# Optimization experiments

Measured on AMD Instinct MI355X. Metric: run time of the kernel, lower is better.

## Reference

```python
import jax, jax.numpy as jnp
import numpy as np

DEPTH = 10
N_VARS = 2
BATCH = 32768
N_LEAVES = 2 ** DEPTH
N_INTERNAL = N_LEAVES - 1
TAU = 1.0
# fp32 analogues of torch.finfo(float64).eps based guards
EPS = float(np.finfo(np.float32).eps)      # _TERM_EPS / _CHILD_EPS
BYPASS = 1.0 - EPS                          # _BYPASS
CLAMP = 1e30                                # _CLAMP (fp32-safe)
TERM_R, TERM_I = 1.0, 0.0                   # EML terminal '1' -> 1+0j
CHILD_IDX = N_VARS + 1


def setup_inputs() -> dict:
    key = jax.random.key(0)
    k1, k2, k3 = jax.random.split(key, 3)
    x = jax.random.normal(k1, (BATCH, N_VARS), dtype=jnp.float32)
    leaf_logits = jax.random.normal(k2, (N_LEAVES, N_VARS + 1), dtype=jnp.float32)
    leaf_logits = leaf_logits.at[:, 0].add(2.0)
    gate_logits = jax.random.normal(k3, (N_INTERNAL, 2, N_VARS + 2), dtype=jnp.float32)
    gate_logits = gate_logits.at[..., 0].add(4.0)
    return {"x": x, "leaf_logits": leaf_logits, "gate_logits": gate_logits}


def _clamp_complex(z):
    r = jnp.clip(jnp.nan_to_num(z.real, nan=0.0, posinf=CLAMP, neginf=-CLAMP), -CLAMP, CLAMP)
    i = jnp.clip(jnp.nan_to_num(z.imag, nan=0.0, posinf=CLAMP, neginf=-CLAMP), -CLAMP, CLAMP)
    return jax.lax.complex(r, i)


def _blend(ps, child, x_r, x_i):
    # ps: [n_pairs, n_vars+2], child: [B, n_pairs] complex
    p_child = ps[:, CHILD_IDX][None, :]                      # [1, P]
    mask_c = p_child > EPS
    safe_cr = jnp.where(mask_c, child.real, 0.0)
    safe_ci = jnp.where(mask_c, child.imag, 0.0)
    p_child_safe = jnp.where(mask_c, p_child, 0.0)
    p_term = ps[:, 0][None, :]                               # [1, P]
    # variable contributions: [P, V] x [B, V] -> [B, P]
    var_r = jnp.einsum('pv,bv->bp', ps[:, 1:CHILD_IDX], x_r)
    var_i = jnp.einsum('pv,bv->bp', ps[:, 1:CHILD_IDX], x_i)
    blend_r = p_term * TERM_R + p_child_safe * safe_cr + var_r
    blend_i = p_term * TERM_I + p_child_safe * safe_ci + var_i
    # hard bypass when one prob saturates
    b1 = p_term > BYPASS
    blend_r = jnp.where(b1, TERM_R, blend_r)
    blend_i = jnp.where(b1, TERM_I, blend_i)
    for v in range(N_VARS):
        bx = ps[:, v + 1][None, :] > BYPASS
        blend_r = jnp.where(bx, x_r[:, v:v + 1], blend_r)
        blend_i = jnp.where(bx, x_i[:, v:v + 1], blend_i)
    return jax.lax.complex(blend_r, blend_i)


def reference(x, leaf_logits, gate_logits):
    xc = x.astype(jnp.complex64)                              # [B, V]
    batch = x.shape[0]
    w = jax.nn.softmax(leaf_logits / TAU, axis=1).astype(jnp.complex64)  # [L, V+1]
    term_col = jnp.full((batch, 1), TERM_R + 0j, dtype=jnp.complex64)
    candidates = jnp.concatenate([term_col, xc], axis=1)      # [B, V+1]
    level = candidates @ w.T                                  # [B, L]
    gate_probs = jax.nn.softmax(gate_logits / TAU, axis=-1)   # [I, 2, V+2]
    x_r, x_i = x, jnp.zeros_like(x)

    node_idx = 0
    while level.shape[1] > 1:  # static python loop over DEPTH levels
        n_pairs = level.shape[1] // 2
        left = level[:, 0::2]
        right = level[:, 1::2]
        pg = gate_probs[node_idx:node_idx + n_pairs]          # [P, 2, V+2]
        left_in = _blend(pg[:, 0, :], left, x_r, x_i)
        right_in = _blend(pg[:, 1, :], right, x_r, x_i)
        # EML op: eml(a, b) = exp(a) - ln(b)
        level = _clamp_complex(jnp.exp(left_in) - jnp.log(right_in))
        node_idx += n_pairs

    leaf_probs = jax.nn.softmax(leaf_logits / TAU, axis=1)
    return level[:, 0], leaf_probs, gate_probs
```

## Files before the change

kernel.cpp:

```cpp
#include <hip/hip_runtime.h>
#include <math.h>

#define EPSF     1.1920928955078125e-07f
#define BYPASSF  0.9999998807907104f
#define CLAMPF   1e30f
#define NBATCH   32768

#define INV2PI    0.15915494309189535f
#define INV2PI_HI 0.15915493667125701904f
#define INV2PI_LO 6.42063831e-9f
#define L2E       1.4426950408889634f
#define L2E_HI    1.44269502162933349609f
#define L2E_LO    1.92596299e-8f
#define LN2F      0.69314718055994530942f
#define PI_F      3.14159274101257324219f
#define PIO2_F    1.57079637050628662109f

#define SLAB_SRC 504
#define SLAB_LDS 508
#define GDS_FLOATS (16 * SLAB_LDS + 120)
#define LW_F4_STRIDE 65
#define WS_NEED ((4096 + 8184) * 4)

typedef float v2 __attribute__((ext_vector_type(2)));

__device__ __attribute__((noinline)) float2 slow_sincos(float y) {
  return make_float2(sinf(y), cosf(y));
}

__device__ __forceinline__ void softmax3_store(float a, float b, float c, float* out) {
  float m = fmaxf(a, fmaxf(b, c));
  float e0 = expf(a - m), e1 = expf(b - m), e2 = expf(c - m);
  float s = (e0 + e1) + e2;
  out[0] = e0 / s; out[1] = e1 / s; out[2] = e2 / s;
}

__device__ __forceinline__ void softmax4(const float* __restrict__ in, float* out) {
  float a = in[0], b = in[1], c = in[2], d = in[3];
  float m = fmaxf(fmaxf(a, b), fmaxf(c, d));
  float e0 = expf(a - m), e1 = expf(b - m), e2 = expf(c - m), e3 = expf(d - m);
  float s = ((e0 + e1) + e2) + e3;
  out[0] = e0 / s; out[1] = e1 / s; out[2] = e2 / s; out[3] = e3 / s;
}

__device__ __forceinline__ void fold_gate(float* p) {
  if (p[3] <= EPSF) p[3] = 0.0f;
  if (p[0] > BYPASSF)      { p[0]=1.f; p[1]=0.f; p[2]=0.f; p[3]=0.f; }
  else if (p[1] > BYPASSF) { p[0]=0.f; p[1]=1.f; p[2]=0.f; p[3]=0.f; }
  else if (p[2] > BYPASSF) { p[0]=0.f; p[1]=0.f; p[2]=1.f; p[3]=0.f; }
}

__device__ __forceinline__ float exp_core(float xe, int* n_out) {
  float nf = rintf(xe * L2E);
  float f  = fmaf(xe, L2E_HI, -nf);
  f        = fmaf(xe, L2E_LO, f);
  *n_out   = (int)nf;
  return __builtin_amdgcn_exp2f(f);
}

__device__ __forceinline__ v2 combine2(const float* __restrict__ g8, v2 L, v2 R,
                                       float x0, float x1) {
  float4 gl = *(const float4*)(g8);
  float4 gr = *(const float4*)(g8 + 4);
  float cL = fmaf(gl.z, x1, gl.y * x0) + gl.x;
  float cR = fmaf(gr.z, x1, gr.y * x0) + gr.x;
  v2 lin = __builtin_elementwise_fma((v2){gl.w, gl.w}, L, (v2){cL, 0.0f});
  v2 rin = __builtin_elementwise_fma((v2){gr.w, gr.w}, R, (v2){cR, 0.0f});

  float sy, cy;
  {
    float nf = rintf(lin.y * INV2PI);
    float rv = fmaf(lin.y, INV2PI_HI, -nf);
    rv       = fmaf(lin.y, INV2PI_LO, rv);
    sy = __builtin_amdgcn_sinf(rv);
    cy = __builtin_amdgcn_cosf(rv);
    if (fabsf(lin.y) > 20000.0f) { float2 sc = slow_sincos(lin.y); sy = sc.x; cy = sc.y; }
  }

  float xe = fminf(fmaxf(lin.x, -200.0f), 200.0f);
  int ne;
  float eh = exp_core(xe, &ne);
  v2 ecs = (v2){eh, eh} * (v2){cy, sy};
  float er = __builtin_amdgcn_ldexpf(ecs.x, ne);
  float ei = __builtin_amdgcn_ldexpf(ecs.y, ne);

  float ax = fabsf(rin.x), ay = fabsf(rin.y);
  float mx = fmaxf(ax, ay), mn = fminf(ax, ay);
  float s  = (mx == 0.0f) ? 0.0f : mn * __builtin_amdgcn_rcpf(mx);
  float z  = s * s;
  float lr = LN2F * fmaf(0.5f, __builtin_amdgcn_logf(z + 1.0f), __builtin_amdgcn_logf(mx));
  float u =              0.00282363896f;
  u = fmaf(u, z, -0.0159569028f);
  u = fmaf(u, z,  0.0425049886f);
  u = fmaf(u, z, -0.0748900920f);
  u = fmaf(u, z,  0.1063479334f);
  u = fmaf(u, z, -0.1420273631f);
  u = fmaf(u, z,  0.1999269574f);
  u = fmaf(u, z, -0.3333310186f);
  float at = fmaf(s * z, u, s);
  at = (ay > ax)      ? (PIO2_F - at) : at;
  at = (rin.x < 0.0f) ? (PI_F   - at) : at;
  float li = copysignf(at, rin.y);

  v2 d = (v2){er, ei} - (v2){lr, li};
  v2 c = __builtin_elementwise_min(__builtin_elementwise_max(d, (v2)(-CLAMPF)), (v2)(CLAMPF));
  v2 o;
  o.x = (d.x != d.x) ? 0.0f : c.x;
  o.y = (d.y != d.y) ? 0.0f : c.y;
  return o;
}

__device__ __forceinline__ v2 combine_l1(const float* __restrict__ g8, float Lr, float Rr,
                                         float x0, float x1) {
  float4 gl = *(const float4*)(g8);
  float4 gr = *(const float4*)(g8 + 4);
  float lr_ = fmaf(gl.w, Lr, fmaf(gl.z, x1, gl.y * x0) + gl.x);
  float rr_ = fmaf(gr.w, Rr, fmaf(gr.z, x1, gr.y * x0) + gr.x);

  float xe = fminf(fmaxf(lr_, -200.0f), 200.0f);
  int ne;
  float eh = exp_core(xe, &ne);
  float er = __builtin_amdgcn_ldexpf(eh, ne);

  float lr = LN2F * __builtin_amdgcn_logf(fabsf(rr_));
  v2 o;
  o.x = fminf(fmaxf(er - lr, -CLAMPF), CLAMPF);
  o.y = (rr_ < 0.0f) ? -PI_F : 0.0f;
  return o;
}

__device__ __forceinline__ v2 quartet(const float* __restrict__ bp, const float4* __restrict__ lq,
                                      float x0, float x1) {
  float4 w0 = lq[0], w1 = lq[1], w2 = lq[2], w3 = lq[3];
  float a0 = fmaf(w0.z, x1, fmaf(w0.y, x0, w0.x));
  float a1 = fmaf(w1.z, x1, fmaf(w1.y, x0, w1.x));
  float a2 = fmaf(w2.z, x1, fmaf(w2.y, x0, w2.x));
  float a3 = fmaf(w3.z, x1, fmaf(w3.y, x0, w3.x));
  v2 c01 = combine_l1(bp + 0, a0, a1, x0, x1);
  v2 c23 = combine_l1(bp + 8, a2, a3, x0, x1);
  return combine2(bp + 16, c01, c23, x0, x1);
}

__global__ __launch_bounds__(256) void prep_kernel(
    const float* __restrict__ leaf_logits,
    const float* __restrict__ gate_logits,
    float* __restrict__ out_leaf,
    float* __restrict__ out_gate,
    float* __restrict__ ws_leaf,
    float* __restrict__ ws_gate) {
  int i = blockIdx.x * 256 + threadIdx.x;
  if (i < 1024) {
    float p[3];
    softmax3_store(leaf_logits[i * 3], leaf_logits[i * 3 + 1], leaf_logits[i * 3 + 2], p);
    out_leaf[i * 3] = p[0]; out_leaf[i * 3 + 1] = p[1]; out_leaf[i * 3 + 2] = p[2];
    ((float4*)ws_leaf)[i] = make_float4(p[0], p[1], p[2], 0.0f);
  } else if (i < 1024 + 2046) {
    int j = i - 1024;
    int g = j >> 1, half = j & 1;
    float p[4];
    softmax4(gate_logits + j * 4, p);
    ((float4*)out_gate)[j] = make_float4(p[0], p[1], p[2], p[3]);
    fold_gate(p);
    int di;
    if (g < 1008) {
      int z  = 1024 - g;
      int k  = __clz(z - 1) - 21;
      int pp = g - (1024 - (2048 >> k));
      int t  = pp >> (6 - k);
      int pl = pp & ((1 << (6 - k)) - 1);
      int L  = ((pl + 1) << k) - 1;
      int step = L - __popc(L) + (k - 1);
      di = t * SLAB_SRC + step * 8;
    } else {
      di = 16 * SLAB_SRC + (g - 1008) * 8;
    }
    ((float4*)(ws_gate + di))[half] = make_float4(p[0], p[1], p[2], p[3]);
  }
}

__global__ __launch_bounds__(1024, 2) void tree16_kernel(
    const float* __restrict__ x,
    const float* __restrict__ ws_leaf,
    const float* __restrict__ ws_gate,
    float* __restrict__ out0, int cplx) {

  __shared__ __align__(16) float gds[GDS_FLOATS];
  __shared__ __align__(16) float lwds[16 * LW_F4_STRIDE * 4];
  const int tid = threadIdx.x;

  {
    float4* g4 = (float4*)gds;
    const float4* s4 = (const float4*)ws_gate;
    for (int c = tid; c < 2016; c += 1024) {
      int t = c / 126;
      int r = c - t * 126;
      g4[t * 127 + r] = s4[c];
    }
    if (tid < 30) g4[2032 + tid] = s4[2016 + tid];
    float4* l4 = (float4*)lwds;
    const float4* sl = (const float4*)ws_leaf;
    l4[tid + (tid >> 6)] = sl[tid];
  }
  __syncthreads();

  const int gtid = blockIdx.x * 1024 + tid;
  const int e  = gtid >> 4;
  const int lt = tid & 15;
  const float2 xv = ((const float2*)x)[e];
  const float x0 = xv.x, x1 = xv.y;
  const float* gb  = &gds[lt * SLAB_LDS];
  const float* tds = &gds[16 * SLAB_LDS];
  const float4* lwp = (const float4*)lwds + lt * LW_F4_STRIDE;

  v2 p4, p5, p6;
  v2 res = (v2)(0.0f);
  int off = 0;

  #pragma unroll 1
  for (int h2 = 0; h2 < 8; ++h2) {
    const float* bp = gb + off;
    const float4* lq = lwp + 8 * h2;
    v2 c03 = quartet(bp +  0, lq,     x0, x1);
    v2 c47 = quartet(bp + 24, lq + 4, x0, x1);
    v2 cur = combine2(bp + 48, c03, c47, x0, x1);
    if (!(h2 & 1)) { p4 = cur; }
    else {
      cur = combine2(bp + 56, p4, cur, x0, x1);
      if (!(h2 & 2)) { p5 = cur; }
      else {
        cur = combine2(bp + 64, p5, cur, x0, x1);
        if (!(h2 & 4)) { p6 = cur; }
        else           { res = combine2(bp + 72, p6, cur, x0, x1); }
      }
    }
    off = (8 * (h2 + 1) - __popc(h2 + 1)) * 8;
  }

  v2 v = res;
  { v2 o; o.x = __shfl_xor(v.x, 1); o.y = __shfl_xor(v.y, 1);
    v2 L, R;
    L.x = (lt & 1) ? o.x : v.x; L.y = (lt & 1) ? o.y : v.y;
    R.x = (lt & 1) ? v.x : o.x; R.y = (lt & 1) ? v.y : o.y;
    v = combine2(tds + (lt >> 1) * 8, L, R, x0, x1); }
  { v2 o; o.x = __shfl_xor(v.x, 2); o.y = __shfl_xor(v.y, 2);
    v2 L, R;
    L.x = (lt & 2) ? o.x : v.x; L.y = (lt & 2) ? o.y : v.y;
    R.x = (lt & 2) ? v.x : o.x; R.y = (lt & 2) ? v.y : o.y;
    v = combine2(tds + (8 + (lt >> 2)) * 8, L, R, x0, x1); }
  { v2 o; o.x = __shfl_xor(v.x, 4); o.y = __shfl_xor(v.y, 4);
    v2 L, R;
    L.x = (lt & 4) ? o.x : v.x; L.y = (lt & 4) ? o.y : v.y;
    R.x = (lt & 4) ? v.x : o.x; R.y = (lt & 4) ? v.y : o.y;
    v = combine2(tds + (12 + (lt >> 3)) * 8, L, R, x0, x1); }
  { v2 o; o.x = __shfl_xor(v.x, 8); o.y = __shfl_xor(v.y, 8);
    v2 L, R;
    L.x = (lt & 8) ? o.x : v.x; L.y = (lt & 8) ? o.y : v.y;
    R.x = (lt & 8) ? v.x : o.x; R.y = (lt & 8) ? v.y : o.y;
    v = combine2(tds + 14 * 8, L, R, x0, x1); }

  if (lt == 0) {
    if (cplx) { out0[2 * e] = v.x; out0[2 * e + 1] = v.y; }
    else      { out0[e] = v.x; }
  }
}

#define GSTRIDE  1020
#define LSTRIDE  516

__device__ __forceinline__ void store_gate_fb(const float* __restrict__ in, float* __restrict__ out) {
  float p[4];
  softmax4(in, p);
  fold_gate(p);
  out[0]=p[0]; out[1]=p[1]; out[2]=p[2]; out[3]=p[3];
}

__global__ __launch_bounds__(512) void tree_fb_kernel(
    const float* __restrict__ x,
    const float* __restrict__ leaf_logits,
    const float* __restrict__ gate_logits,
    float* __restrict__ out0, int cplx) {

  __shared__ __align__(16) float gds[8 * GSTRIDE];
  __shared__ __align__(16) float tds[7 * 8];
  __shared__ __align__(16) float lw[8 * LSTRIDE];
  const int tid = threadIdx.x;

  for (int l = tid; l < 1024; l += 512) {
    float p[3];
    softmax3_store(leaf_logits[l * 3], leaf_logits[l * 3 + 1], leaf_logits[l * 3 + 2], p);
    *(float4*)&lw[(l >> 7) * LSTRIDE + (l & 127) * 4] = make_float4(p[0], p[1], p[2], 0.0f);
  }
  for (int g = tid; g < 1016; g += 512) {
    int z  = 1024 - g;
    int k  = __clz(z - 1) - 21;
    int p  = g - (1024 - (2048 >> k));
    int t  = p >> (7 - k);
    int pl = p & ((1 << (7 - k)) - 1);
    int L  = ((pl + 1) << k) - 1;
    int step = L - __popc(L) + (k - 1);
    float* dst = &gds[t * GSTRIDE + step * 8];
    store_gate_fb(gate_logits + g * 8,     dst);
    store_gate_fb(gate_logits + g * 8 + 4, dst + 4);
  }
  if (tid < 7) {
    int g = 1016 + tid;
    store_gate_fb(gate_logits + g * 8,     &tds[tid * 8]);
    store_gate_fb(gate_logits + g * 8 + 4, &tds[tid * 8 + 4]);
  }
  __syncthreads();

  const int gtid = blockIdx.x * 512 + tid;
  const int e  = gtid >> 3;
  const int lt = tid & 7;
  const float2 xv = ((const float2*)x)[e];
  const float x0 = xv.x, x1 = xv.y;
  const float* gb = &gds[lt * GSTRIDE];
  const float* lb = &lw[lt * LSTRIDE];

  v2 p1, p2, p3, p4, p5, p6;
  v2 res = (v2)(0.0f);
  int step = 0;

  #pragma unroll 2
  for (int h = 0; h < 64; ++h) {
    float4 w0 = *(const float4*)&lb[(2 * h) * 4];
    float4 w1 = *(const float4*)&lb[(2 * h + 1) * 4];
    float a = fmaf(w0.z, x1, fmaf(w0.y, x0, w0.x));
    float b = fmaf(w1.z, x1, fmaf(w1.y, x0, w1.x));
    v2 cur = combine_l1(gb + step * 8, a, b, x0, x1); step++;
    if (!(h & 1))  { p1 = cur; continue; }
    cur = combine2(gb + step * 8, p1, cur, x0, x1); step++;
    if (!(h & 2))  { p2 = cur; continue; }
    cur = combine2(gb + step * 8, p2, cur, x0, x1); step++;
    if (!(h & 4))  { p3 = cur; continue; }
    cur = combine2(gb + step * 8, p3, cur, x0, x1); step++;
    if (!(h & 8))  { p4 = cur; continue; }
    cur = combine2(gb + step * 8, p4, cur, x0, x1); step++;
    if (!(h & 16)) { p5 = cur; continue; }
    cur = combine2(gb + step * 8, p5, cur, x0, x1); step++;
    if (!(h & 32)) { p6 = cur; continue; }
    cur = combine2(gb + step * 8, p6, cur, x0, x1); step++;
    res = cur;
  }

  v2 v = res;
  { v2 o; o.x = __shfl_xor(v.x, 1); o.y = __shfl_xor(v.y, 1);
    v2 L, R;
    L.x = (lt & 1) ? o.x : v.x; L.y = (lt & 1) ? o.y : v.y;
    R.x = (lt & 1) ? v.x : o.x; R.y = (lt & 1) ? v.y : o.y;
    v = combine2(&tds[(lt >> 1) * 8], L, R, x0, x1); }
  { v2 o; o.x = __shfl_xor(v.x, 2); o.y = __shfl_xor(v.y, 2);
    v2 L, R;
    L.x = (lt & 2) ? o.x : v.x; L.y = (lt & 2) ? o.y : v.y;
    R.x = (lt & 2) ? v.x : o.x; R.y = (lt & 2) ? v.y : o.y;
    v = combine2(&tds[(4 + (lt >> 2)) * 8], L, R, x0, x1); }
  { v2 o; o.x = __shfl_xor(v.x, 4); o.y = __shfl_xor(v.y, 4);
    v2 L, R;
    L.x = (lt & 4) ? o.x : v.x; L.y = (lt & 4) ? o.y : v.y;
    R.x = (lt & 4) ? v.x : o.x; R.y = (lt & 4) ? v.y : o.y;
    v = combine2(&tds[6 * 8], L, R, x0, x1); }

  if (lt == 0) {
    if (cplx) { out0[2 * e] = v.x; out0[2 * e + 1] = v.y; }
    else      { out0[e] = v.x; }
  }
}

__global__ __launch_bounds__(256) void probs_fb_kernel(
    const float* __restrict__ leaf_logits,
    const float* __restrict__ gate_logits,
    float* __restrict__ out_leaf,
    float* __restrict__ out_gate) {
  int i = blockIdx.x * 256 + threadIdx.x;
  if (i < 1024) {
    softmax3_store(leaf_logits[i * 3], leaf_logits[i * 3 + 1], leaf_logits[i * 3 + 2],
                   &out_leaf[i * 3]);
  } else if (i < 1024 + 2046) {
    int j = i - 1024;
    float p[4];
    softmax4(gate_logits + j * 4, p);
    ((float4*)out_gate)[j] = make_float4(p[0], p[1], p[2], p[3]);
  }
}

extern "C" void kernel_launch(void* const* d_in, const int* in_sizes, int n_in,
                              void* d_out, int out_size, void* d_ws, size_t ws_size,
                              hipStream_t stream) {
  const float* x  = (const float*)d_in[0];
  const float* ll = (const float*)d_in[1];
  const float* gl = (const float*)d_in[2];
  float* out0 = (float*)d_out;

  int S = out_size - (3072 + 8184);
  int cplx = (S >= 2 * NBATCH) ? 1 : 0;
  float* out_leaf = out0 + S;
  float* out_gate = out_leaf + 3072;

  if (ws_size >= (size_t)WS_NEED) {
    float* ws_leaf = (float*)d_ws;
    float* ws_gate = ws_leaf + 4096;
    prep_kernel<<<12, 256, 0, stream>>>(ll, gl, out_leaf, out_gate, ws_leaf, ws_gate);
    tree16_kernel<<<512, 1024, 0, stream>>>(x, ws_leaf, ws_gate, out0, cplx);
  } else {
    tree_fb_kernel<<<512, 512, 0, stream>>>(x, ll, gl, out0, cplx);
    probs_fb_kernel<<<12, 256, 0, stream>>>(ll, gl, out_leaf, out_gate);
  }
}
```

Measured before the change: 55.57 us.

## Process two batch elements per thread with packed float2 math in tree kernel

New measurement: 50.93 us. 1.09x faster.

```diff
diff --git a/kernel.cpp b/kernel.cpp
--- a/kernel.cpp
+++ b/kernel.cpp
@@ -24,6 +24,12 @@
 
 typedef float v2 __attribute__((ext_vector_type(2)));
 
+__device__ __forceinline__ v2 pkfma(v2 a, v2 b, v2 c) {
+  return __builtin_elementwise_fma(a, b, c);
+}
+
+struct C2p { v2 r, i; };
+
 __device__ __attribute__((noinline)) float2 slow_sincos(float y) {
   return make_float2(sinf(y), cosf(y));
 }
@@ -50,95 +56,120 @@
   else if (p[2] > BYPASSF) { p[0]=0.f; p[1]=0.f; p[2]=1.f; p[3]=0.f; }
 }
 
-__device__ __forceinline__ float exp_core(float xe, int* n_out) {
-  float nf = rintf(xe * L2E);
-  float f  = fmaf(xe, L2E_HI, -nf);
-  f        = fmaf(xe, L2E_LO, f);
-  *n_out   = (int)nf;
-  return __builtin_amdgcn_exp2f(f);
-}
-
-__device__ __forceinline__ v2 combine2(const float* __restrict__ g8, v2 L, v2 R,
-                                       float x0, float x1) {
+
+__device__ __forceinline__ C2p combine2p(const float* __restrict__ g8, C2p L, C2p R,
+                                         v2 x0, v2 x1) {
   float4 gl = *(const float4*)(g8);
   float4 gr = *(const float4*)(g8 + 4);
-  float cL = fmaf(gl.z, x1, gl.y * x0) + gl.x;
-  float cR = fmaf(gr.z, x1, gr.y * x0) + gr.x;
-  v2 lin = __builtin_elementwise_fma((v2){gl.w, gl.w}, L, (v2){cL, 0.0f});
-  v2 rin = __builtin_elementwise_fma((v2){gr.w, gr.w}, R, (v2){cR, 0.0f});
-
-  float sy, cy;
+  v2 cL = pkfma((v2)(gl.z), x1, (v2)(gl.y) * x0) + (v2)(gl.x);
+  v2 cR = pkfma((v2)(gr.z), x1, (v2)(gr.y) * x0) + (v2)(gr.x);
+  v2 linr = pkfma((v2)(gl.w), L.r, cL);
+  v2 lini = (v2)(gl.w) * L.i;
+  v2 rinr = pkfma((v2)(gr.w), R.r, cR);
+  v2 rini = (v2)(gr.w) * R.i;
+
+  v2 sy, cy;
   {
-    float nf = rintf(lin.y * INV2PI);
-    float rv = fmaf(lin.y, INV2PI_HI, -nf);
-    rv       = fmaf(lin.y, INV2PI_LO, rv);
-    sy = __builtin_amdgcn_sinf(rv);
-    cy = __builtin_amdgcn_cosf(rv);
-    if (fabsf(lin.y) > 20000.0f) { float2 sc = slow_sincos(lin.y); sy = sc.x; cy = sc.y; }
-  }
-
-  float xe = fminf(fmaxf(lin.x, -200.0f), 200.0f);
-  int ne;
-  float eh = exp_core(xe, &ne);
-  v2 ecs = (v2){eh, eh} * (v2){cy, sy};
-  float er = __builtin_amdgcn_ldexpf(ecs.x, ne);
-  float ei = __builtin_amdgcn_ldexpf(ecs.y, ne);
-
-  float ax = fabsf(rin.x), ay = fabsf(rin.y);
-  float mx = fmaxf(ax, ay), mn = fminf(ax, ay);
-  float s  = (mx == 0.0f) ? 0.0f : mn * __builtin_amdgcn_rcpf(mx);
-  float z  = s * s;
-  float lr = LN2F * fmaf(0.5f, __builtin_amdgcn_logf(z + 1.0f), __builtin_amdgcn_logf(mx));
-  float u =              0.00282363896f;
-  u = fmaf(u, z, -0.0159569028f);
-  u = fmaf(u, z,  0.0425049886f);
-  u = fmaf(u, z, -0.0748900920f);
-  u = fmaf(u, z,  0.1063479334f);
-  u = fmaf(u, z, -0.1420273631f);
-  u = fmaf(u, z,  0.1999269574f);
-  u = fmaf(u, z, -0.3333310186f);
-  float at = fmaf(s * z, u, s);
-  at = (ay > ax)      ? (PIO2_F - at) : at;
-  at = (rin.x < 0.0f) ? (PI_F   - at) : at;
-  float li = copysignf(at, rin.y);
-
-  v2 d = (v2){er, ei} - (v2){lr, li};
-  v2 c = __builtin_elementwise_min(__builtin_elementwise_max(d, (v2)(-CLAMPF)), (v2)(CLAMPF));
-  v2 o;
-  o.x = (d.x != d.x) ? 0.0f : c.x;
-  o.y = (d.y != d.y) ? 0.0f : c.y;
+    v2 t = lini * (v2)(INV2PI);
+    v2 nf; nf.x = rintf(t.x); nf.y = rintf(t.y);
+    v2 rv = pkfma(lini, (v2)(INV2PI_HI), -nf);
+    rv     = pkfma(lini, (v2)(INV2PI_LO), rv);
+    sy.x = __builtin_amdgcn_sinf(rv.x); sy.y = __builtin_amdgcn_sinf(rv.y);
+    cy.x = __builtin_amdgcn_cosf(rv.x); cy.y = __builtin_amdgcn_cosf(rv.y);
+    if (fabsf(lini.x) > 20000.0f) { float2 sc = slow_sincos(lini.x); sy.x = sc.x; cy.x = sc.y; }
+    if (fabsf(lini.y) > 20000.0f) { float2 sc = slow_sincos(lini.y); sy.y = sc.x; cy.y = sc.y; }
+  }
+
+  v2 xe; xe.x = __builtin_amdgcn_fmed3f(linr.x, -200.0f, 200.0f);
+         xe.y = __builtin_amdgcn_fmed3f(linr.y, -200.0f, 200.0f);
+  v2 t2 = xe * (v2)(L2E);
+  v2 nfe; nfe.x = rintf(t2.x); nfe.y = rintf(t2.y);
+  v2 f = pkfma(xe, (v2)(L2E_HI), -nfe);
+  f     = pkfma(xe, (v2)(L2E_LO), f);
+  v2 eh; eh.x = __builtin_amdgcn_exp2f(f.x); eh.y = __builtin_amdgcn_exp2f(f.y);
+  int ne0 = (int)nfe.x, ne1 = (int)nfe.y;
+  v2 ecr = eh * cy, eci = eh * sy;
+  v2 er, ei;
+  er.x = __builtin_amdgcn_ldexpf(ecr.x, ne0); er.y = __builtin_amdgcn_ldexpf(ecr.y, ne1);
+  ei.x = __builtin_amdgcn_ldexpf(eci.x, ne0); ei.y = __builtin_amdgcn_ldexpf(eci.y, ne1);
+
+  v2 mx, mn;
+  mx.x = fmaxf(fabsf(rinr.x), fabsf(rini.x)); mx.y = fmaxf(fabsf(rinr.y), fabsf(rini.y));
+  mn.x = fminf(fabsf(rinr.x), fabsf(rini.x)); mn.y = fminf(fabsf(rinr.y), fabsf(rini.y));
+  v2 rc; rc.x = __builtin_amdgcn_rcpf(mx.x); rc.y = __builtin_amdgcn_rcpf(mx.y);
+  v2 s = mn * rc;
+  s.x = (mx.x == 0.0f) ? 0.0f : s.x;
+  s.y = (mx.y == 0.0f) ? 0.0f : s.y;
+  v2 z = s * s;
+  v2 lga; lga.x = __builtin_amdgcn_logf(z.x + 1.0f); lga.y = __builtin_amdgcn_logf(z.y + 1.0f);
+  v2 lgm; lgm.x = __builtin_amdgcn_logf(mx.x);       lgm.y = __builtin_amdgcn_logf(mx.y);
+  v2 lr = (v2)(LN2F) * pkfma((v2)(0.5f), lga, lgm);
+  v2 u = (v2)(0.00282363896f);
+  u = pkfma(u, z, (v2)(-0.0159569028f));
+  u = pkfma(u, z, (v2)( 0.0425049886f));
+  u = pkfma(u, z, (v2)(-0.0748900920f));
+  u = pkfma(u, z, (v2)( 0.1063479334f));
+  u = pkfma(u, z, (v2)(-0.1420273631f));
+  u = pkfma(u, z, (v2)( 0.1999269574f));
+  u = pkfma(u, z, (v2)(-0.3333310186f));
+  v2 at = pkfma(s * z, u, s);
+  v2 q1 = (v2)(PIO2_F) - at;
+  at.x = (fabsf(rini.x) > fabsf(rinr.x)) ? q1.x : at.x;
+  at.y = (fabsf(rini.y) > fabsf(rinr.y)) ? q1.y : at.y;
+  v2 q2 = (v2)(PI_F) - at;
+  at.x = (rinr.x < 0.0f) ? q2.x : at.x;
+  at.y = (rinr.y < 0.0f) ? q2.y : at.y;
+  v2 li; li.x = copysignf(at.x, rini.x); li.y = copysignf(at.y, rini.y);
+
+  v2 dre = er - lr, dim = ei - li;
+  v2 cre = __builtin_elementwise_min(__builtin_elementwise_max(dre, (v2)(-CLAMPF)), (v2)(CLAMPF));
+  v2 cim = __builtin_elementwise_min(__builtin_elementwise_max(dim, (v2)(-CLAMPF)), (v2)(CLAMPF));
+  C2p o;
+  o.r.x = (dre.x != dre.x) ? 0.0f : cre.x;
+  o.r.y = (dre.y != dre.y) ? 0.0f : cre.y;
+  o.i.x = (dim.x != dim.x) ? 0.0f : cim.x;
+  o.i.y = (dim.y != dim.y) ? 0.0f : cim.y;
   return o;
 }
 
-__device__ __forceinline__ v2 combine_l1(const float* __restrict__ g8, float Lr, float Rr,
-                                         float x0, float x1) {
+__device__ __forceinline__ C2p combine_l1p(const float* __restrict__ g8, v2 Lr, v2 Rr,
+                                           v2 x0, v2 x1) {
   float4 gl = *(const float4*)(g8);
   float4 gr = *(const float4*)(g8 + 4);
-  float lr_ = fmaf(gl.w, Lr, fmaf(gl.z, x1, gl.y * x0) + gl.x);
-  float rr_ = fmaf(gr.w, Rr, fmaf(gr.z, x1, gr.y * x0) + gr.x);
-
-  float xe = fminf(fmaxf(lr_, -200.0f), 200.0f);
-  int ne;
-  float eh = exp_core(xe, &ne);
-  float er = __builtin_amdgcn_ldexpf(eh, ne);
-
-  float lr = LN2F * __builtin_amdgcn_logf(fabsf(rr_));
-  v2 o;
-  o.x = fminf(fmaxf(er - lr, -CLAMPF), CLAMPF);
-  o.y = (rr_ < 0.0f) ? -PI_F : 0.0f;
+  v2 lr_ = pkfma((v2)(gl.w), Lr, pkfma((v2)(gl.z), x1, (v2)(gl.y) * x0) + (v2)(gl.x));
+  v2 rr_ = pkfma((v2)(gr.w), Rr, pkfma((v2)(gr.z), x1, (v2)(gr.y) * x0) + (v2)(gr.x));
+
+  v2 xe; xe.x = __builtin_amdgcn_fmed3f(lr_.x, -200.0f, 200.0f);
+         xe.y = __builtin_amdgcn_fmed3f(lr_.y, -200.0f, 200.0f);
+  v2 t2 = xe * (v2)(L2E);
+  v2 nfe; nfe.x = rintf(t2.x); nfe.y = rintf(t2.y);
+  v2 f = pkfma(xe, (v2)(L2E_HI), -nfe);
+  f     = pkfma(xe, (v2)(L2E_LO), f);
+  v2 eh; eh.x = __builtin_amdgcn_exp2f(f.x); eh.y = __builtin_amdgcn_exp2f(f.y);
+  v2 er;
+  er.x = __builtin_amdgcn_ldexpf(eh.x, (int)nfe.x);
+  er.y = __builtin_amdgcn_ldexpf(eh.y, (int)nfe.y);
+
+  v2 lg; lg.x = __builtin_amdgcn_logf(fabsf(rr_.x)); lg.y = __builtin_amdgcn_logf(fabsf(rr_.y));
+  v2 d = er - (v2)(LN2F) * lg;
+  C2p o;
+  o.r.x = __builtin_amdgcn_fmed3f(d.x, -CLAMPF, CLAMPF);
+  o.r.y = __builtin_amdgcn_fmed3f(d.y, -CLAMPF, CLAMPF);
+  o.i.x = (rr_.x < 0.0f) ? -PI_F : 0.0f;
+  o.i.y = (rr_.y < 0.0f) ? -PI_F : 0.0f;
   return o;
 }
 
-__device__ __forceinline__ v2 quartet(const float* __restrict__ bp, const float4* __restrict__ lq,
-                                      float x0, float x1) {
+__device__ __forceinline__ C2p quartetp(const float* __restrict__ bp, const float4* __restrict__ lq,
+                                        v2 x0, v2 x1) {
   float4 w0 = lq[0], w1 = lq[1], w2 = lq[2], w3 = lq[3];
-  float a0 = fmaf(w0.z, x1, fmaf(w0.y, x0, w0.x));
-  float a1 = fmaf(w1.z, x1, fmaf(w1.y, x0, w1.x));
-  float a2 = fmaf(w2.z, x1, fmaf(w2.y, x0, w2.x));
-  float a3 = fmaf(w3.z, x1, fmaf(w3.y, x0, w3.x));
-  v2 c01 = combine_l1(bp + 0, a0, a1, x0, x1);
-  v2 c23 = combine_l1(bp + 8, a2, a3, x0, x1);
-  return combine2(bp + 16, c01, c23, x0, x1);
+  v2 a0 = pkfma((v2)(w0.z), x1, pkfma((v2)(w0.y), x0, (v2)(w0.x)));
+  v2 a1 = pkfma((v2)(w1.z), x1, pkfma((v2)(w1.y), x0, (v2)(w1.x)));
+  v2 a2 = pkfma((v2)(w2.z), x1, pkfma((v2)(w2.y), x0, (v2)(w2.x)));
+  v2 a3 = pkfma((v2)(w3.z), x1, pkfma((v2)(w3.y), x0, (v2)(w3.x)));
+  C2p c01 = combine_l1p(bp + 0, a0, a1, x0, x1);
+  C2p c23 = combine_l1p(bp + 8, a2, a3, x0, x1);
+  return combine2p(bp + 16, c01, c23, x0, x1);
 }
 
 __global__ __launch_bounds__(256) void prep_kernel(
@@ -178,7 +209,7 @@
   }
 }
 
-__global__ __launch_bounds__(1024, 2) void tree16_kernel(
+__global__ __launch_bounds__(1024, 1) void tree16p_kernel(
     const float* __restrict__ x,
     const float* __restrict__ ws_leaf,
     const float* __restrict__ ws_gate,
@@ -204,68 +235,157 @@
   __syncthreads();
 
   const int gtid = blockIdx.x * 1024 + tid;
-  const int e  = gtid >> 4;
+  const int pe = gtid >> 4;
   const int lt = tid & 15;
-  const float2 xv = ((const float2*)x)[e];
-  const float x0 = xv.x, x1 = xv.y;
+  const float4 xw = ((const float4*)x)[pe];
+  v2 x0, x1;
+  x0.x = xw.x; x0.y = xw.z;
+  x1.x = xw.y; x1.y = xw.w;
   const float* gb  = &gds[lt * SLAB_LDS];
   const float* tds = &gds[16 * SLAB_LDS];
   const float4* lwp = (const float4*)lwds + lt * LW_F4_STRIDE;
 
-  v2 p4, p5, p6;
-  v2 res = (v2)(0.0f);
+  C2p p4, p5, p6;
+  C2p res; res.r = (v2)(0.0f); res.i = (v2)(0.0f);
   int off = 0;
 
   #pragma unroll 1
   for (int h2 = 0; h2 < 8; ++h2) {
     const float* bp = gb + off;
     const float4* lq = lwp + 8 * h2;
-    v2 c03 = quartet(bp +  0, lq,     x0, x1);
-    v2 c47 = quartet(bp + 24, lq + 4, x0, x1);
-    v2 cur = combine2(bp + 48, c03, c47, x0, x1);
+    C2p c03 = quartetp(bp +  0, lq,     x0, x1);
+    C2p c47 = quartetp(bp + 24, lq + 4, x0, x1);
+    C2p cur = combine2p(bp + 48, c03, c47, x0, x1);
     if (!(h2 & 1)) { p4 = cur; }
     else {
-      cur = combine2(bp + 56, p4, cur, x0, x1);
+      cur = combine2p(bp + 56, p4, cur, x0, x1);
       if (!(h2 & 2)) { p5 = cur; }
       else {
-        cur = combine2(bp + 64, p5, cur, x0, x1);
+        cur = combine2p(bp + 64, p5, cur, x0, x1);
         if (!(h2 & 4)) { p6 = cur; }
-        else           { res = combine2(bp + 72, p6, cur, x0, x1); }
+        else           { res = combine2p(bp + 72, p6, cur, x0, x1); }
       }
     }
     off = (8 * (h2 + 1) - __popc(h2 + 1)) * 8;
   }
 
-  v2 v = res;
-  { v2 o; o.x = __shfl_xor(v.x, 1); o.y = __shfl_xor(v.y, 1);
-    v2 L, R;
-    L.x = (lt & 1) ? o.x : v.x; L.y = (lt & 1) ? o.y : v.y;
-    R.x = (lt & 1) ? v.x : o.x; R.y = (lt & 1) ? v.y : o.y;
-    v = combine2(tds + (lt >> 1) * 8, L, R, x0, x1); }
-  { v2 o; o.x = __shfl_xor(v.x, 2); o.y = __shfl_xor(v.y, 2);
-    v2 L, R;
-    L.x = (lt & 2) ? o.x : v.x; L.y = (lt & 2) ? o.y : v.y;
-    R.x = (lt & 2) ? v.x : o.x; R.y = (lt & 2) ? v.y : o.y;
-    v = combine2(tds + (8 + (lt >> 2)) * 8, L, R, x0, x1); }
-  { v2 o; o.x = __shfl_xor(v.x, 4); o.y = __shfl_xor(v.y, 4);
-    v2 L, R;
-    L.x = (lt & 4) ? o.x : v.x; L.y = (lt & 4) ? o.y : v.y;
-    R.x = (lt & 4) ? v.x : o.x; R.y = (lt & 4) ? v.y : o.y;
-    v = combine2(tds + (12 + (lt >> 3)) * 8, L, R, x0, x1); }
-  { v2 o; o.x = __shfl_xor(v.x, 8); o.y = __shfl_xor(v.y, 8);
-    v2 L, R;
-    L.x = (lt & 8) ? o.x : v.x; L.y = (lt & 8) ? o.y : v.y;
-    R.x = (lt & 8) ? v.x : o.x; R.y = (lt & 8) ? v.y : o.y;
-    v = combine2(tds + 14 * 8, L, R, x0, x1); }
+  C2p v = res;
+  { C2p o;
+    o.r.x = __shfl_xor(v.r.x, 1); o.r.y = __shfl_xor(v.r.y, 1);
+    o.i.x = __shfl_xor(v.i.x, 1); o.i.y = __shfl_xor(v.i.y, 1);
+    bool sw = (lt & 1);
+    C2p L, R;
+    L.r = sw ? o.r : v.r; L.i = sw ? o.i : v.i;
+    R.r = sw ? v.r : o.r; R.i = sw ? v.i : o.i;
+    v = combine2p(tds + (lt >> 1) * 8, L, R, x0, x1); }
+  { C2p o;
+    o.r.x = __shfl_xor(v.r.x, 2); o.r.y = __shfl_xor(v.r.y, 2);
+    o.i.x = __shfl_xor(v.i.x, 2); o.i.y = __shfl_xor(v.i.y, 2);
+    bool sw = (lt & 2);
+    C2p L, R;
+    L.r = sw ? o.r : v.r; L.i = sw ? o.i : v.i;
+    R.r = sw ? v.r : o.r; R.i = sw ? v.i : o.i;
+    v = combine2p(tds + (8 + (lt >> 2)) * 8, L, R, x0, x1); }
+  { C2p o;
+    o.r.x = __shfl_xor(v.r.x, 4); o.r.y = __shfl_xor(v.r.y, 4);
+    o.i.x = __shfl_xor(v.i.x, 4); o.i.y = __shfl_xor(v.i.y, 4);
+    bool sw = (lt & 4);
+    C2p L, R;
+    L.r = sw ? o.r : v.r; L.i = sw ? o.i : v.i;
+    R.r = sw ? v.r : o.r; R.i = sw ? v.i : o.i;
+    v = combine2p(tds + (12 + (lt >> 3)) * 8, L, R, x0, x1); }
+  { C2p o;
+    o.r.x = __shfl_xor(v.r.x, 8); o.r.y = __shfl_xor(v.r.y, 8);
+    o.i.x = __shfl_xor(v.i.x, 8); o.i.y = __shfl_xor(v.i.y, 8);
+    bool sw = (lt & 8);
+    C2p L, R;
+    L.r = sw ? o.r : v.r; L.i = sw ? o.i : v.i;
+    R.r = sw ? v.r : o.r; R.i = sw ? v.i : o.i;
+    v = combine2p(tds + 14 * 8, L, R, x0, x1); }
 
   if (lt == 0) {
-    if (cplx) { out0[2 * e] = v.x; out0[2 * e + 1] = v.y; }
-    else      { out0[e] = v.x; }
+    if (cplx) {
+      ((float4*)out0)[pe] = make_float4(v.r.x, v.i.x, v.r.y, v.i.y);
+    } else {
+      ((float2*)out0)[pe] = make_float2(v.r.x, v.r.y);
+    }
   }
 }
 
 #define GSTRIDE  1020
 #define LSTRIDE  516
+
+__device__ __forceinline__ v2 combine2(const float* __restrict__ g8, v2 L, v2 R,
+                                       float x0, float x1) {
+  float4 gl = *(const float4*)(g8);
+  float4 gr = *(const float4*)(g8 + 4);
+  float cL = fmaf(gl.z, x1, gl.y * x0) + gl.x;
+  float cR = fmaf(gr.z, x1, gr.y * x0) + gr.x;
+  v2 glw; glw.x = gl.w; glw.y = gl.w;
+  v2 grw; grw.x = gr.w; grw.y = gr.w;
+  v2 cLv; cLv.x = cL; cLv.y = 0.0f;
+  v2 cRv; cRv.x = cR; cRv.y = 0.0f;
+  v2 lin = pkfma(glw, L, cLv);
+  v2 rin = pkfma(grw, R, cRv);
+  float sy, cy;
+  {
+    float nf = rintf(lin.y * INV2PI);
+    float rv = fmaf(lin.y, INV2PI_HI, -nf);
+    rv       = fmaf(lin.y, INV2PI_LO, rv);
+    sy = __builtin_amdgcn_sinf(rv);
+    cy = __builtin_amdgcn_cosf(rv);
+    if (fabsf(lin.y) > 20000.0f) { float2 sc = slow_sincos(lin.y); sy = sc.x; cy = sc.y; }
+  }
+  float xe = fminf(fmaxf(lin.x, -200.0f), 200.0f);
+  float nfe = rintf(xe * L2E);
+  float f  = fmaf(xe, L2E_HI, -nfe);
+  f        = fmaf(xe, L2E_LO, f);
+  float eh = __builtin_amdgcn_exp2f(f);
+  int ne = (int)nfe;
+  float er = __builtin_amdgcn_ldexpf(eh * cy, ne);
+  float ei = __builtin_amdgcn_ldexpf(eh * sy, ne);
+  float ax = fabsf(rin.x), ay = fabsf(rin.y);
+  float mx = fmaxf(ax, ay), mn = fminf(ax, ay);
+  float s  = (mx == 0.0f) ? 0.0f : mn * __builtin_amdgcn_rcpf(mx);
+  float z  = s * s;
+  float lr = LN2F * fmaf(0.5f, __builtin_amdgcn_logf(z + 1.0f), __builtin_amdgcn_logf(mx));
+  float u =              0.00282363896f;
+  u = fmaf(u, z, -0.0159569028f);
+  u = fmaf(u, z,  0.0425049886f);
+  u = fmaf(u, z, -0.0748900920f);
+  u = fmaf(u, z,  0.1063479334f);
+  u = fmaf(u, z, -0.1420273631f);
+  u = fmaf(u, z,  0.1999269574f);
+  u = fmaf(u, z, -0.3333310186f);
+  float at = fmaf(s * z, u, s);
+  at = (ay > ax)      ? (PIO2_F - at) : at;
+  at = (rin.x < 0.0f) ? (PI_F   - at) : at;
+  float li = copysignf(at, rin.y);
+  float dx = er - lr, dy = ei - li;
+  v2 o;
+  o.x = (dx != dx) ? 0.0f : __builtin_amdgcn_fmed3f(dx, -CLAMPF, CLAMPF);
+  o.y = (dy != dy) ? 0.0f : __builtin_amdgcn_fmed3f(dy, -CLAMPF, CLAMPF);
+  return o;
+}
+
+__device__ __forceinline__ v2 combine_l1(const float* __restrict__ g8, float Lr, float Rr,
+                                         float x0, float x1) {
+  float4 gl = *(const float4*)(g8);
+  float4 gr = *(const float4*)(g8 + 4);
+  float lr_ = fmaf(gl.w, Lr, fmaf(gl.z, x1, gl.y * x0) + gl.x);
+  float rr_ = fmaf(gr.w, Rr, fmaf(gr.z, x1, gr.y * x0) + gr.x);
+  float xe = fminf(fmaxf(lr_, -200.0f), 200.0f);
+  float nfe = rintf(xe * L2E);
+  float f  = fmaf(xe, L2E_HI, -nfe);
+  f        = fmaf(xe, L2E_LO, f);
+  float eh = __builtin_amdgcn_exp2f(f);
+  float er = __builtin_amdgcn_ldexpf(eh, (int)nfe);
+  float lr = LN2F * __builtin_amdgcn_logf(fabsf(rr_));
+  v2 o;
+  o.x = fminf(fmaxf(er - lr, -CLAMPF), CLAMPF);
+  o.y = (rr_ < 0.0f) ? -PI_F : 0.0f;
+  return o;
+}
 
 __device__ __forceinline__ void store_gate_fb(const float* __restrict__ in, float* __restrict__ out) {
   float p[4];
@@ -400,7 +520,7 @@
     float* ws_leaf = (float*)d_ws;
     float* ws_gate = ws_leaf + 4096;
     prep_kernel<<<12, 256, 0, stream>>>(ll, gl, out_leaf, out_gate, ws_leaf, ws_gate);
-    tree16_kernel<<<512, 1024, 0, stream>>>(x, ws_leaf, ws_gate, out0, cplx);
+    tree16p_kernel<<<256, 1024, 0, stream>>>(x, ws_leaf, ws_gate, out0, cplx);
   } else {
     tree_fb_kernel<<<512, 512, 0, stream>>>(x, ll, gl, out0, cplx);
     probs_fb_kernel<<<12, 256, 0, stream>>>(ll, gl, out_leaf, out_gate);
```
